# Performance work log

Measured on AMD Instinct MI355X. Metric: run time of the kernel, lower is better.

Reference implementation:

```python
import jax, jax.numpy as jnp
import numpy as np

N, C, D, H, W = 4, 9, 16, 1024, 1024  # batch, grid channels, grid size, image HxW


def setup_inputs() -> dict:
    key = jax.random.key(0)
    k1, k2, k3, k4 = jax.random.split(key, 4)
    bilateral_grid = jax.random.normal(k1, (N, C, D, D, D), dtype=jnp.float32)
    guidemap = jax.random.uniform(k2, (N, 3, H, W), dtype=jnp.float32)
    conv_w = jax.random.normal(k3, (3, C + 3), dtype=jnp.float32) * 0.1  # 1x1 conv kernel
    conv_b = jax.random.normal(k4, (3,), dtype=jnp.float32) * 0.1
    return {"bilateral_grid": bilateral_grid, "guidemap": guidemap,
            "conv_w": conv_w, "conv_b": conv_b}


def _trilinear_slice(grid, guide):
    # grid: [N, C, D, D, D]; guide: [N, 3, H, W] with values in [0,1]
    n, c, d = grid.shape[0], grid.shape[1], grid.shape[2]
    h, w = guide.shape[2], guide.shape[3]
    grid_flat = grid.reshape(n, c, d * d * d)
    coords = jnp.clip(guide, 0.0, 1.0) * (d - 1)          # [N,3,H,W]
    i0 = jnp.clip(jnp.floor(coords), 0, d - 2).astype(jnp.int32)
    f = coords - i0.astype(coords.dtype)                   # fractional part
    r0, g0, b0 = i0[:, 0], i0[:, 1], i0[:, 2]              # [N,H,W]
    fr, fg, fb = f[:, 0], f[:, 1], f[:, 2]                 # [N,H,W]

    def gather(ir, ig, ib):
        flat = ((ir * d + ig) * d + ib).reshape(n, 1, h * w)
        return jnp.take_along_axis(grid_flat, flat, axis=2)  # [N,C,H*W]

    out = jnp.zeros((n, c, h * w), dtype=grid.dtype)
    for dr in (0, 1):
        for dg in (0, 1):
            for db in (0, 1):
                wgt = ((fr if dr else 1.0 - fr) *
                       (fg if dg else 1.0 - fg) *
                       (fb if db else 1.0 - fb)).reshape(n, 1, h * w)
                out = out + gather(r0 + dr, g0 + dg, b0 + db) * wgt
    return out.reshape(n, c, h, w)


def reference(bilateral_grid, guidemap, conv_w, conv_b):
    res = _trilinear_slice(bilateral_grid, guidemap)       # [N,9,H,W]
    res = jnp.concatenate([res, guidemap], axis=1)         # [N,12,H,W]
    out = jnp.einsum('oi,nihw->nohw', conv_w, res) + conv_b[None, :, None, None]
    return out
```

## Files before the change

kernel.cpp:

```cpp
#include <hip/hip_runtime.h>
#include <hip/hip_bf16.h>

static constexpr int N_ = 4;
static constexpr int C_ = 9;
static constexpr int D_ = 16;
static constexpr int HWp = 1024 * 1024;
static constexpr int CELLS = D_ * D_ * D_;
static constexpr int PT = HWp / 4;
static constexpr int TPB = 512;
static constexpr int BPI = 256;

__device__ __forceinline__ void unpack3(uint2 w, float& x, float& y, float& z) {
    x = __uint_as_float(w.x << 16);
    y = __uint_as_float(w.x & 0xFFFF0000u);
    z = __uint_as_float(w.y << 16);
}

__device__ __forceinline__ float lerp1(float a, float b, float t) {
    return fmaf(b - a, t, a);
}

__global__ __launch_bounds__(TPB) void slice_kernel(
    const float* __restrict__ grid, const float* __restrict__ guide,
    const float* __restrict__ cw, const float* __restrict__ cbias,
    float* __restrict__ out)
{
    __shared__ uint2 sPre[CELLS];

    const int n  = blockIdx.x >> 8;
    const int bi = blockIdx.x & (BPI - 1);

    {
        const float* g = grid + (size_t)n * C_ * CELLS;
#pragma unroll
        for (int k = 0; k < CELLS / TPB; ++k) {
            int cell = k * TPB + threadIdx.x;
            float a0 = 0.f, a1 = 0.f, a2 = 0.f;
#pragma unroll
            for (int c = 0; c < C_; ++c) {
                float v = g[(size_t)c * CELLS + cell];
                a0 = fmaf(cw[c], v, a0);
                a1 = fmaf(cw[12 + c], v, a1);
                a2 = fmaf(cw[24 + c], v, a2);
            }
            unsigned short b0 = __bfloat16_as_ushort(__float2bfloat16(a0));
            unsigned short b1 = __bfloat16_as_ushort(__float2bfloat16(a1));
            unsigned short b2 = __bfloat16_as_ushort(__float2bfloat16(a2));
            uint2 v;
            v.x = (unsigned)b0 | ((unsigned)b1 << 16);
            v.y = (unsigned)b2;
            sPre[cell] = v;
        }
    }
    __syncthreads();

    const float4* gR = (const float4*)(guide + (size_t)(n * 3 + 0) * HWp);
    const float4* gG = (const float4*)(guide + (size_t)(n * 3 + 1) * HWp);
    const float4* gB = (const float4*)(guide + (size_t)(n * 3 + 2) * HWp);
    float4* oR = (float4*)(out + (size_t)(n * 3 + 0) * HWp);
    float4* oG = (float4*)(out + (size_t)(n * 3 + 1) * HWp);
    float4* oB = (float4*)(out + (size_t)(n * 3 + 2) * HWp);

    const float w0r = cw[9],  w0g = cw[10], w0b = cw[11];
    const float w1r = cw[21], w1g = cw[22], w1b = cw[23];
    const float w2r = cw[33], w2g = cw[34], w2b = cw[35];
    const float bi0 = cbias[0], bi1 = cbias[1], bi2 = cbias[2];

    const int base0 = bi * (PT / BPI);

#pragma unroll
    for (int it = 0; it < (PT / BPI) / TPB; ++it) {
        const int p4 = base0 + it * TPB + threadIdx.x;
        float4 r4 = gR[p4];
        float4 g4 = gG[p4];
        float4 b4 = gB[p4];

        float rr[4] = {r4.x, r4.y, r4.z, r4.w};
        float gg[4] = {g4.x, g4.y, g4.z, g4.w};
        float bb[4] = {b4.x, b4.y, b4.z, b4.w};
        float o0[4], o1[4], o2[4];

#pragma unroll
        for (int j = 0; j < 4; ++j) {
            float cr = fminf(fmaxf(rr[j], 0.f), 1.f) * 15.f;
            float cg = fminf(fmaxf(gg[j], 0.f), 1.f) * 15.f;
            float cb = fminf(fmaxf(bb[j], 0.f), 1.f) * 15.f;
            int ir = min((int)cr, 14);
            int ig = min((int)cg, 14);
            int ib = min((int)cb, 14);
            float fr = cr - (float)ir;
            float fg = cg - (float)ig;
            float fb = cb - (float)ib;
            int base = (ir * 16 + ig) * 16 + ib;

            uint2 q000 = sPre[base];
            uint2 q001 = sPre[base + 1];
            uint2 q010 = sPre[base + 16];
            uint2 q011 = sPre[base + 17];
            uint2 q100 = sPre[base + 256];
            uint2 q101 = sPre[base + 257];
            uint2 q110 = sPre[base + 272];
            uint2 q111 = sPre[base + 273];

            float ax, ay, az, bx, by, bz;
            float v00x, v00y, v00z, v01x, v01y, v01z;
            float v10x, v10y, v10z, v11x, v11y, v11z;

            unpack3(q000, ax, ay, az); unpack3(q001, bx, by, bz);
            v00x = lerp1(ax, bx, fb); v00y = lerp1(ay, by, fb); v00z = lerp1(az, bz, fb);
            unpack3(q010, ax, ay, az); unpack3(q011, bx, by, bz);
            v01x = lerp1(ax, bx, fb); v01y = lerp1(ay, by, fb); v01z = lerp1(az, bz, fb);
            unpack3(q100, ax, ay, az); unpack3(q101, bx, by, bz);
            v10x = lerp1(ax, bx, fb); v10y = lerp1(ay, by, fb); v10z = lerp1(az, bz, fb);
            unpack3(q110, ax, ay, az); unpack3(q111, bx, by, bz);
            v11x = lerp1(ax, bx, fb); v11y = lerp1(ay, by, fb); v11z = lerp1(az, bz, fb);

            float v0x = lerp1(v00x, v01x, fg);
            float v0y = lerp1(v00y, v01y, fg);
            float v0z = lerp1(v00z, v01z, fg);
            float v1x = lerp1(v10x, v11x, fg);
            float v1y = lerp1(v10y, v11y, fg);
            float v1z = lerp1(v10z, v11z, fg);

            float vx = lerp1(v0x, v1x, fr);
            float vy = lerp1(v0y, v1y, fr);
            float vz = lerp1(v0z, v1z, fr);

            o0[j] = vx + fmaf(w0r, rr[j], fmaf(w0g, gg[j], fmaf(w0b, bb[j], bi0)));
            o1[j] = vy + fmaf(w1r, rr[j], fmaf(w1g, gg[j], fmaf(w1b, bb[j], bi1)));
            o2[j] = vz + fmaf(w2r, rr[j], fmaf(w2g, gg[j], fmaf(w2b, bb[j], bi2)));
        }

        oR[p4] = make_float4(o0[0], o0[1], o0[2], o0[3]);
        oG[p4] = make_float4(o1[0], o1[1], o1[2], o1[3]);
        oB[p4] = make_float4(o2[0], o2[1], o2[2], o2[3]);
    }
}

extern "C" void kernel_launch(void* const* d_in, const int* in_sizes, int n_in,
                              void* d_out, int out_size, void* d_ws, size_t ws_size,
                              hipStream_t stream) {
    const float* grid  = (const float*)d_in[0];
    const float* guide = (const float*)d_in[1];
    const float* cw    = (const float*)d_in[2];
    const float* cb    = (const float*)d_in[3];
    float* out = (float*)d_out;

    slice_kernel<<<N_ * BPI, TPB, 0, stream>>>(grid, guide, cw, cb, out);
}
```

Before: 116.3 us.

## Precompute folded grid in separate kernel and use nontemporal guide/output access

```diff
diff --git a/kernel.cpp b/kernel.cpp
--- a/kernel.cpp
+++ b/kernel.cpp
@@ -10,6 +10,8 @@
 static constexpr int TPB = 512;
 static constexpr int BPI = 256;
 
+typedef float f32x4 __attribute__((ext_vector_type(4)));
+
 __device__ __forceinline__ void unpack3(uint2 w, float& x, float& y, float& z) {
     x = __uint_as_float(w.x << 16);
     y = __uint_as_float(w.x & 0xFFFF0000u);
@@ -20,8 +22,32 @@
     return fmaf(b - a, t, a);
 }
 
+__global__ __launch_bounds__(256) void fold_kernel(
+    const float* __restrict__ grid, const float* __restrict__ cw,
+    uint2* __restrict__ folded)
+{
+    const int idx  = blockIdx.x * 256 + threadIdx.x;
+    const int n    = idx >> 12;
+    const int cell = idx & (CELLS - 1);
+    const float* g = grid + (size_t)n * C_ * CELLS + cell;
+
+    float a0 = 0.f, a1 = 0.f, a2 = 0.f;
+#pragma unroll
+    for (int c = 0; c < C_; ++c) {
+        float v = g[(size_t)c * CELLS];
+        a0 = fmaf(cw[c],      v, a0);
+        a1 = fmaf(cw[12 + c], v, a1);
+        a2 = fmaf(cw[24 + c], v, a2);
+    }
+    uint2 v;
+    v.x = (unsigned)__bfloat16_as_ushort(__float2bfloat16(a0))
+        | ((unsigned)__bfloat16_as_ushort(__float2bfloat16(a1)) << 16);
+    v.y = (unsigned)__bfloat16_as_ushort(__float2bfloat16(a2));
+    folded[idx] = v;
+}
+
 __global__ __launch_bounds__(TPB) void slice_kernel(
-    const float* __restrict__ grid, const float* __restrict__ guide,
+    const uint2* __restrict__ folded, const float* __restrict__ guide,
     const float* __restrict__ cw, const float* __restrict__ cbias,
     float* __restrict__ out)
 {
@@ -31,35 +57,22 @@
     const int bi = blockIdx.x & (BPI - 1);
 
     {
-        const float* g = grid + (size_t)n * C_ * CELLS;
+        const uint4* src = (const uint4*)(folded + (size_t)n * CELLS);
+        uint4* dst = (uint4*)sPre;
 #pragma unroll
-        for (int k = 0; k < CELLS / TPB; ++k) {
-            int cell = k * TPB + threadIdx.x;
-            float a0 = 0.f, a1 = 0.f, a2 = 0.f;
-#pragma unroll
-            for (int c = 0; c < C_; ++c) {
-                float v = g[(size_t)c * CELLS + cell];
-                a0 = fmaf(cw[c], v, a0);
-                a1 = fmaf(cw[12 + c], v, a1);
-                a2 = fmaf(cw[24 + c], v, a2);
-            }
-            unsigned short b0 = __bfloat16_as_ushort(__float2bfloat16(a0));
-            unsigned short b1 = __bfloat16_as_ushort(__float2bfloat16(a1));
-            unsigned short b2 = __bfloat16_as_ushort(__float2bfloat16(a2));
-            uint2 v;
-            v.x = (unsigned)b0 | ((unsigned)b1 << 16);
-            v.y = (unsigned)b2;
-            sPre[cell] = v;
+        for (int k = 0; k < (CELLS / 2) / TPB; ++k) {
+            int i = k * TPB + threadIdx.x;
+            dst[i] = src[i];
         }
     }
     __syncthreads();
 
-    const float4* gR = (const float4*)(guide + (size_t)(n * 3 + 0) * HWp);
-    const float4* gG = (const float4*)(guide + (size_t)(n * 3 + 1) * HWp);
-    const float4* gB = (const float4*)(guide + (size_t)(n * 3 + 2) * HWp);
-    float4* oR = (float4*)(out + (size_t)(n * 3 + 0) * HWp);
-    float4* oG = (float4*)(out + (size_t)(n * 3 + 1) * HWp);
-    float4* oB = (float4*)(out + (size_t)(n * 3 + 2) * HWp);
+    const f32x4* gR = (const f32x4*)(guide + (size_t)(n * 3 + 0) * HWp);
+    const f32x4* gG = (const f32x4*)(guide + (size_t)(n * 3 + 1) * HWp);
+    const f32x4* gB = (const f32x4*)(guide + (size_t)(n * 3 + 2) * HWp);
+    f32x4* oR = (f32x4*)(out + (size_t)(n * 3 + 0) * HWp);
+    f32x4* oG = (f32x4*)(out + (size_t)(n * 3 + 1) * HWp);
+    f32x4* oB = (f32x4*)(out + (size_t)(n * 3 + 2) * HWp);
 
     const float w0r = cw[9],  w0g = cw[10], w0b = cw[11];
     const float w1r = cw[21], w1g = cw[22], w1b = cw[23];
@@ -71,9 +84,9 @@
 #pragma unroll
     for (int it = 0; it < (PT / BPI) / TPB; ++it) {
         const int p4 = base0 + it * TPB + threadIdx.x;
-        float4 r4 = gR[p4];
-        float4 g4 = gG[p4];
-        float4 b4 = gB[p4];
+        f32x4 r4 = __builtin_nontemporal_load(gR + p4);
+        f32x4 g4 = __builtin_nontemporal_load(gG + p4);
+        f32x4 b4 = __builtin_nontemporal_load(gB + p4);
 
         float rr[4] = {r4.x, r4.y, r4.z, r4.w};
         float gg[4] = {g4.x, g4.y, g4.z, g4.w};
@@ -131,9 +144,12 @@
             o2[j] = vz + fmaf(w2r, rr[j], fmaf(w2g, gg[j], fmaf(w2b, bb[j], bi2)));
         }
 
-        oR[p4] = make_float4(o0[0], o0[1], o0[2], o0[3]);
-        oG[p4] = make_float4(o1[0], o1[1], o1[2], o1[3]);
-        oB[p4] = make_float4(o2[0], o2[1], o2[2], o2[3]);
+        f32x4 s0 = {o0[0], o0[1], o0[2], o0[3]};
+        f32x4 s1 = {o1[0], o1[1], o1[2], o1[3]};
+        f32x4 s2 = {o2[0], o2[1], o2[2], o2[3]};
+        __builtin_nontemporal_store(s0, oR + p4);
+        __builtin_nontemporal_store(s1, oG + p4);
+        __builtin_nontemporal_store(s2, oB + p4);
     }
 }
 
@@ -145,6 +161,8 @@
     const float* cw    = (const float*)d_in[2];
     const float* cb    = (const float*)d_in[3];
     float* out = (float*)d_out;
+    uint2* folded = (uint2*)d_ws;
 
-    slice_kernel<<<N_ * BPI, TPB, 0, stream>>>(grid, guide, cw, cb, out);
+    fold_kernel<<<(N_ * CELLS) / 256, 256, 0, stream>>>(grid, cw, folded);
+    slice_kernel<<<N_ * BPI, TPB, 0, stream>>>(folded, guide, cw, cb, out);
 }
```

Result: no change. 115.2 us (-0.9%).
